# Optimization experiments

Hardware: AMD Instinct MI355X
Metric: run time of the kernel (lower is better)

## Reference

```python
import jax, jax.numpy as jnp
import numpy as np

POOL_SIZES = (1, 3, 6, 8)
EPS = 1e-5


def conv1x1(x, W, b):
    # x: [b, cin, h, w], W: [cout, cin], b: [cout]
    return jnp.einsum('bchw,oc->bohw', x, W) + b[None, :, None, None]


def ppm(x):
    # x: [b, c, h, w] -> [b, c, S] with S = sum(p*p); H,W divisible by each p
    b, c, h, w = x.shape
    outs = []
    for p in POOL_SIZES:
        pooled = x.reshape(b, c, p, h // p, p, w // p).mean(axis=(3, 5))
        outs.append(pooled.reshape(b, c, p * p))
    return jnp.concatenate(outs, axis=-1)


def setup_inputs() -> dict:
    key = jax.random.key(0)
    ks = jax.random.split(key, 8)
    B, Cin, H, W = 4, 512, 120, 120
    Ck, Cv, Cout = 256, 256, 512
    x = jax.random.normal(ks[0], (B, Cin, H, W), dtype=jnp.float32)
    sc = lambda cin: 1.0 / np.sqrt(cin)
    Wk = jax.random.normal(ks[1], (Ck, Cin), dtype=jnp.float32) * sc(Cin)
    bk = jnp.zeros((Ck,), jnp.float32)
    gamma = jnp.ones((Ck,), jnp.float32)
    beta = jnp.zeros((Ck,), jnp.float32)
    mean = jax.random.normal(ks[2], (Ck,), dtype=jnp.float32) * 0.1
    var = jax.random.uniform(ks[3], (Ck,), dtype=jnp.float32, minval=0.5, maxval=1.5)
    Wv = jax.random.normal(ks[4], (Cv, Cin), dtype=jnp.float32) * sc(Cin)
    bv = jnp.zeros((Cv,), jnp.float32)
    # original inits Conv_Out to zero; use random weights for a nontrivial baseline
    Wo = jax.random.normal(ks[5], (Cout, Cv), dtype=jnp.float32) * sc(Cv)
    bo = jnp.zeros((Cout,), jnp.float32)
    return {'x': x, 'Wk': Wk, 'bk': bk, 'gamma': gamma, 'beta': beta,
            'mean': mean, 'var': var, 'Wv': Wv, 'bv': bv, 'Wo': Wo, 'bo': bo}


def reference(x, Wk, bk, gamma, beta, mean, var, Wv, bv, Wo, bo):
    b, _, h, w = x.shape
    ck = Wk.shape[0]
    cv = Wv.shape[0]
    # shared Conv_Key / Conv_Query: conv1x1 -> BN (inference) -> ReLU
    kq = conv1x1(x, Wk, bk)
    inv = gamma / jnp.sqrt(var + EPS)
    kq = jax.nn.relu(kq * inv[None, :, None, None] + (beta - mean * inv)[None, :, None, None])
    value = ppm(conv1x1(x, Wv, bv)).transpose(0, 2, 1)      # [b, S, cv]
    key = ppm(kq)                                            # [b, ck, S]
    query = kq.reshape(b, ck, h * w).transpose(0, 2, 1)      # [b, hw, ck]
    scores = jnp.einsum('bnc,bcs->bns', query, key) * (ck ** -0.5)
    attn = jax.nn.softmax(scores, axis=-1)                   # [b, hw, S]
    agg = jnp.einsum('bns,bsv->bnv', attn, value)            # [b, hw, cv]
    agg = agg.transpose(0, 2, 1).reshape(b, cv, h, w)
    return conv1x1(agg, Wo, bo)
```

## Files before the change

kernel.cpp:

```cpp
#include <hip/hip_runtime.h>
#include <cstdint>
#include <cstddef>

#define HW 14400
#define WIDTH 120
#define S_TOT 110

typedef unsigned short u16;
typedef __attribute__((ext_vector_type(8))) short bf16x8;
typedef __attribute__((ext_vector_type(4))) float f32x4;

__device__ __forceinline__ u16 f2bf(float x) {
  unsigned u = __float_as_uint(x);
  unsigned r = (u + 0x7fffu + ((u >> 16) & 1u)) >> 16;
  return (u16)r;
}
__device__ __forceinline__ float bf2f(u16 h) {
  return __uint_as_float((unsigned)h << 16);
}

__device__ __forceinline__ void async16(void* lds, const void* g) {
  __builtin_amdgcn_global_load_lds(
      (const __attribute__((address_space(1))) void*)g,
      (__attribute__((address_space(3))) void*)lds, 16, 0, 0);
}

__global__ __launch_bounds__(256) void pool_kernel(const float* __restrict__ in,
                                                   float* __restrict__ outp) {
  __shared__ float part[576];
  const float* plane = in + (size_t)blockIdx.x * HW;
  int t = threadIdx.x;
  for (int bb = t; bb < 576; bb += 256) {
    int by = bb / 24, bx = bb % 24;
    const float* p0 = plane + (by * 5) * WIDTH + bx * 5;
    float s = 0.f;
#pragma unroll
    for (int yy = 0; yy < 5; ++yy)
#pragma unroll
      for (int xx = 0; xx < 5; ++xx) s += p0[yy * WIDTH + xx];
    part[bb] = s;
  }
  __syncthreads();
  if (t < S_TOT) {
    float s = 0.f;
    if (t == 0) {
      for (int i = 0; i < 576; ++i) s += part[i];
      s *= (1.f / 14400.f);
    } else if (t < 10) {
      int idx = t - 1, i = idx / 3, j = idx % 3;
      for (int a = 0; a < 8; ++a)
        for (int c = 0; c < 8; ++c) s += part[(i * 8 + a) * 24 + (j * 8 + c)];
      s *= (1.f / 1600.f);
    } else if (t < 46) {
      int idx = t - 10, i = idx / 6, j = idx % 6;
      for (int a = 0; a < 4; ++a)
        for (int c = 0; c < 4; ++c) s += part[(i * 4 + a) * 24 + (j * 4 + c)];
      s *= (1.f / 400.f);
    } else {
      int idx = t - 46, i = idx / 8, j = idx % 8;
      for (int a = 0; a < 3; ++a)
        for (int c = 0; c < 3; ++c) s += part[(i * 3 + a) * 24 + (j * 3 + c)];
      s *= (1.f / 225.f);
    }
    outp[(size_t)blockIdx.x * S_TOT + t] = s;
  }
}

__global__ __launch_bounds__(256) void convert_w(const float* __restrict__ in,
                                                 u16* __restrict__ hi,
                                                 u16* __restrict__ lo, int n) {
  int i = blockIdx.x * 256 + threadIdx.x;
  if (i < n) {
    float v = in[i];
    u16 h = f2bf(v);
    hi[i] = h;
    lo[i] = f2bf(v - bf2f(h));
  }
}

__global__ __launch_bounds__(256) void convert_x(const float* __restrict__ X,
                                                 u16* __restrict__ xth,
                                                 u16* __restrict__ xtl) {
  __shared__ float ls[64][65];
  int b = blockIdx.z;
  int n0 = blockIdx.x * 64, k0 = blockIdx.y * 64;
  int t = threadIdx.x;
  int rt = t >> 4, c4 = (t & 15) * 4;
#pragma unroll
  for (int rr = 0; rr < 4; ++rr) {
    int kk = rr * 16 + rt;
    float4 v = *(const float4*)&X[((size_t)(b * 512 + k0 + kk)) * HW + n0 + c4];
    ls[kk][c4] = v.x; ls[kk][c4 + 1] = v.y; ls[kk][c4 + 2] = v.z; ls[kk][c4 + 3] = v.w;
  }
  __syncthreads();
#pragma unroll
  for (int rr = 0; rr < 4; ++rr) {
    int nn = rr * 16 + rt;
    float v0 = ls[c4 + 0][nn], v1 = ls[c4 + 1][nn], v2 = ls[c4 + 2][nn], v3 = ls[c4 + 3][nn];
    ushort4 oh, ol;
    oh.x = f2bf(v0); ol.x = f2bf(v0 - bf2f(oh.x));
    oh.y = f2bf(v1); ol.y = f2bf(v1 - bf2f(oh.y));
    oh.z = f2bf(v2); ol.z = f2bf(v2 - bf2f(oh.z));
    oh.w = f2bf(v3); ol.w = f2bf(v3 - bf2f(oh.w));
    size_t idx = ((size_t)(b * HW + n0 + nn)) * 512 + k0 + c4;
    *(ushort4*)&xth[idx] = oh;
    *(ushort4*)&xtl[idx] = ol;
  }
}

template <int K, int M_TOT, bool BNRELU>
__global__ __launch_bounds__(256) void gemm_mfma(
    const u16* __restrict__ Ah, const u16* __restrict__ Al,
    const u16* __restrict__ Bh, const u16* __restrict__ Bl,
    float* __restrict__ C,
    const float* __restrict__ p0, const float* __restrict__ p1,
    const float* __restrict__ p2, const float* __restrict__ p3,
    const float* __restrict__ p4) {
  constexpr int NSTEP = K / 32;
  __shared__ alignas(16) u16 sAh[256 * 32];
  __shared__ alignas(16) u16 sAl[256 * 32];
  __shared__ alignas(16) u16 sBh[64 * 32];
  __shared__ alignas(16) u16 sBl[64 * 32];
  __shared__ float sP0[256], sP1[256];

  int t = threadIdx.x, w = t >> 6, l = t & 63;
  int b = blockIdx.z;
  int n0 = blockIdx.x * 64;
  int m0 = blockIdx.y * 256;

  if (BNRELU) {
    int m = m0 + t;
    float iv = p1[m] * rsqrtf(p4[m] + 1e-5f);
    sP0[t] = iv;
    sP1[t] = (p0[m] - p3[m]) * iv + p2[m];
  } else {
    sP0[t] = p0[m0 + t];
  }

  int crow = l >> 2;
  int cbyte = (l & 3) * 16;
  const size_t bOff = (size_t)b * HW;

  f32x4 acc[4][4];
#pragma unroll
  for (int i = 0; i < 4; ++i)
#pragma unroll
    for (int j = 0; j < 4; ++j) acc[i][j] = (f32x4){0.f, 0.f, 0.f, 0.f};

  int fr = l & 15, fk = (l >> 4) * 8;

  for (int ks = 0; ks < NSTEP; ++ks) {
    int k0 = ks * 32;
#pragma unroll
    for (int c = 0; c < 10; ++c) {
      int i = w * 10 + c;
      const u16* g;
      u16* d;
      if (i < 16) {
        g = Ah + (size_t)(m0 + i * 16 + crow) * K + k0;
        d = sAh + i * 512;
      } else if (i < 32) {
        g = Al + (size_t)(m0 + (i - 16) * 16 + crow) * K + k0;
        d = sAl + (i - 16) * 512;
      } else if (i < 36) {
        g = Bh + (bOff + n0 + (i - 32) * 16 + crow) * K + k0;
        d = sBh + (i - 32) * 512;
      } else {
        g = Bl + (bOff + n0 + (i - 36) * 16 + crow) * K + k0;
        d = sBl + (i - 36) * 512;
      }
      async16((char*)d, (const char*)g + cbyte);
    }
    __syncthreads();

    bf16x8 ah[4], al[4], bh[4], bl[4];
#pragma unroll
    for (int mt = 0; mt < 4; ++mt) {
      int r = w * 64 + mt * 16 + fr;
      ah[mt] = *(const bf16x8*)&sAh[r * 32 + fk];
      al[mt] = *(const bf16x8*)&sAl[r * 32 + fk];
    }
#pragma unroll
    for (int nt = 0; nt < 4; ++nt) {
      int r = nt * 16 + fr;
      bh[nt] = *(const bf16x8*)&sBh[r * 32 + fk];
      bl[nt] = *(const bf16x8*)&sBl[r * 32 + fk];
    }
#pragma unroll
    for (int mt = 0; mt < 4; ++mt)
#pragma unroll
      for (int nt = 0; nt < 4; ++nt) {
        acc[mt][nt] = __builtin_amdgcn_mfma_f32_16x16x32_bf16(ah[mt], bh[nt], acc[mt][nt], 0, 0, 0);
        acc[mt][nt] = __builtin_amdgcn_mfma_f32_16x16x32_bf16(ah[mt], bl[nt], acc[mt][nt], 0, 0, 0);
        acc[mt][nt] = __builtin_amdgcn_mfma_f32_16x16x32_bf16(al[mt], bh[nt], acc[mt][nt], 0, 0, 0);
      }
    __syncthreads();
  }

#pragma unroll
  for (int mt = 0; mt < 4; ++mt) {
    int lmBase = w * 64 + mt * 16 + (l >> 4) * 4;
#pragma unroll
    for (int nt = 0; nt < 4; ++nt) {
      int n = n0 + nt * 16 + fr;
#pragma unroll
      for (int r = 0; r < 4; ++r) {
        int lm = lmBase + r;
        float v = acc[mt][nt][r];
        if (BNRELU)
          v = fmaxf(v * sP0[lm] + sP1[lm], 0.f);
        else
          v = v + sP0[lm];
        C[((size_t)(b * M_TOT + m0 + lm)) * HW + n] = v;
      }
    }
  }
}

__global__ __launch_bounds__(256) void value_kernel(
    const float* __restrict__ Wv, const float* __restrict__ xp,
    const float* __restrict__ bv, float* __restrict__ val) {
  int b = blockIdx.x / S_TOT, s = blockIdx.x % S_TOT;
  __shared__ float xs[512];
  int t = threadIdx.x;
  for (int i = t; i < 512; i += 256) xs[i] = xp[((size_t)b * 512 + i) * S_TOT + s];
  __syncthreads();
  float accv = 0.f;
  const float* w = Wv + (size_t)t * 512;
  for (int k = 0; k < 512; k += 4) {
    float4 w4 = *(const float4*)&w[k];
    accv += w4.x * xs[k] + w4.y * xs[k + 1] + w4.z * xs[k + 2] + w4.w * xs[k + 3];
  }
  val[(size_t)blockIdx.x * 256 + t] = accv + bv[t];
}

__global__ __launch_bounds__(256) void attn_kernel(
    const float* __restrict__ kq, const float* __restrict__ keyp,
    const float* __restrict__ value, u16* __restrict__ aggh,
    u16* __restrict__ aggl) {
  __shared__ float sc[64][113];
  __shared__ float qt[32][64];
  __shared__ float kt[32][112];
  __shared__ float red[4][64];
  __shared__ float rinv[64];
  int b = blockIdx.y;
  int pix0 = blockIdx.x * 64;
  int t = threadIdx.x;

  int pi = t & 7;
  int si = t >> 3;
  float a[8][4];
#pragma unroll
  for (int p = 0; p < 8; ++p)
#pragma unroll
    for (int j = 0; j < 4; ++j) a[p][j] = 0.f;

  for (int c0 = 0; c0 < 256; c0 += 32) {
#pragma unroll
    for (int u = 0; u < 2; ++u) {
      int fi = t + u * 256;
      int cc = fi >> 4, p4 = (fi & 15) * 4;
      *(float4*)&qt[cc][p4] =
          *(const float4*)&kq[((size_t)(b * 256 + c0 + cc)) * HW + pix0 + p4];
    }
    for (int i = t; i < 32 * S_TOT; i += 256) {
      int cc = i / S_TOT, ss = i % S_TOT;
      kt[cc][ss] = keyp[((size_t)(b * 256 + c0 + cc)) * S_TOT + ss];
    }
    __syncthreads();
    for (int cc = 0; cc < 32; ++cc) {
      float4 q0 = *(const float4*)&qt[cc][pi * 8];
      float4 q1 = *(const float4*)&qt[cc][pi * 8 + 4];
#pragma unroll
      for (int j = 0; j < 4; ++j) {
        int s = si + 32 * j;
        if (s < S_TOT) {
          float kv = kt[cc][s];
          a[0][j] += q0.x * kv; a[1][j] += q0.y * kv;
          a[2][j] += q0.z * kv; a[3][j] += q0.w * kv;
          a[4][j] += q1.x * kv; a[5][j] += q1.y * kv;
          a[6][j] += q1.z * kv; a[7][j] += q1.w * kv;
        }
      }
    }
    __syncthreads();
  }
#pragma unroll
  for (int j = 0; j < 4; ++j) {
    int s = si + 32 * j;
    if (s < S_TOT) {
#pragma unroll
      for (int p = 0; p < 8; ++p) sc[pi * 8 + p][s] = a[p][j] * 0.0625f;
    }
  }
  __syncthreads();

  int part = t >> 6, r = t & 63;
  int sbeg = part * 28, send = sbeg + 28 < S_TOT ? sbeg + 28 : S_TOT;
  float mx = -1e30f;
  for (int s = sbeg; s < send; ++s) mx = fmaxf(mx, sc[r][s]);
  red[part][r] = mx;
  __syncthreads();
  float m = fmaxf(fmaxf(red[0][r], red[1][r]), fmaxf(red[2][r], red[3][r]));
  float sum = 0.f;
  for (int s = sbeg; s < send; ++s) {
    float e = __expf(sc[r][s] - m);
    sc[r][s] = e;
    sum += e;
  }
  __syncthreads();
  red[part][r] = sum;
  __syncthreads();
  if (part == 0) rinv[r] = 1.f / (red[0][r] + red[1][r] + red[2][r] + red[3][r]);
  __syncthreads();

  int tn2 = t & 63, tm2 = t >> 6;
  int cv = tn2 * 4;
  float4 acc4[16];
#pragma unroll
  for (int p = 0; p < 16; ++p) acc4[p] = make_float4(0.f, 0.f, 0.f, 0.f);
  const float* vb = value + (size_t)b * S_TOT * 256 + cv;
  for (int s = 0; s < S_TOT; ++s) {
    float4 v4 = *(const float4*)&vb[(size_t)s * 256];
#pragma unroll
    for (int p = 0; p < 16; ++p) {
      float e = sc[tm2 * 16 + p][s];
      acc4[p].x += e * v4.x; acc4[p].y += e * v4.y;
      acc4[p].z += e * v4.z; acc4[p].w += e * v4.w;
    }
  }
#pragma unroll
  for (int p = 0; p < 16; ++p) {
    int pix = tm2 * 16 + p;
    float iv = rinv[pix];
    float v0 = acc4[p].x * iv, v1 = acc4[p].y * iv, v2 = acc4[p].z * iv, v3 = acc4[p].w * iv;
    ushort4 oh, ol;
    oh.x = f2bf(v0); ol.x = f2bf(v0 - bf2f(oh.x));
    oh.y = f2bf(v1); ol.y = f2bf(v1 - bf2f(oh.y));
    oh.z = f2bf(v2); ol.z = f2bf(v2 - bf2f(oh.z));
    oh.w = f2bf(v3); ol.w = f2bf(v3 - bf2f(oh.w));
    size_t base = ((size_t)(b * HW + pix0 + pix)) * 256 + cv;
    *(ushort4*)&aggh[base] = oh;
    *(ushort4*)&aggl[base] = ol;
  }
}

extern "C" void kernel_launch(void* const* d_in, const int* in_sizes, int n_in,
                              void* d_out, int out_size, void* d_ws, size_t ws_size,
                              hipStream_t stream) {
  (void)in_sizes; (void)n_in; (void)out_size; (void)ws_size;
  const float* x     = (const float*)d_in[0];
  const float* Wk    = (const float*)d_in[1];
  const float* bk    = (const float*)d_in[2];
  const float* gamma = (const float*)d_in[3];
  const float* beta  = (const float*)d_in[4];
  const float* mean  = (const float*)d_in[5];
  const float* var   = (const float*)d_in[6];
  const float* Wv    = (const float*)d_in[7];
  const float* bv    = (const float*)d_in[8];
  const float* Wo    = (const float*)d_in[9];
  const float* bo    = (const float*)d_in[10];
  float* out = (float*)d_out;

  char* p = (char*)d_ws;
  float* kq = (float*)p;      p += (size_t)14745600 * 4;
  u16* xth = (u16*)p;         p += (size_t)29491200 * 2;
  u16* xtl = (u16*)p;         p += (size_t)29491200 * 2;
  u16* wkh = (u16*)p;         p += 131072 * 2;
  u16* wkl = (u16*)p;         p += 131072 * 2;
  u16* woh = (u16*)p;         p += 131072 * 2;
  u16* wol = (u16*)p;         p += 131072 * 2;
  float* xp = (float*)p;      p += (size_t)4 * 512 * 110 * 4;
  float* value = (float*)p;   p += (size_t)4 * 110 * 256 * 4;
  float* keyp = (float*)p;    p += (size_t)4 * 256 * 110 * 4;
  u16* aggh = xth;
  u16* aggl = xtl;

  convert_w<<<512, 256, 0, stream>>>(Wk, wkh, wkl, 256 * 512);
  convert_w<<<512, 256, 0, stream>>>(Wo, woh, wol, 512 * 256);
  convert_x<<<dim3(225, 8, 4), 256, 0, stream>>>(x, xth, xtl);
  pool_kernel<<<dim3(4 * 512), dim3(256), 0, stream>>>(x, xp);
  value_kernel<<<dim3(4 * S_TOT), dim3(256), 0, stream>>>(Wv, xp, bv, value);
  gemm_mfma<512, 256, true><<<dim3(225, 1, 4), 256, 0, stream>>>(
      wkh, wkl, xth, xtl, kq, bk, gamma, beta, mean, var);
  pool_kernel<<<dim3(4 * 256), dim3(256), 0, stream>>>(kq, keyp);
  attn_kernel<<<dim3(225, 4), 256, 0, stream>>>(kq, keyp, value, aggh, aggl);
  gemm_mfma<256, 512, false><<<dim3(225, 2, 4), 256, 0, stream>>>(
      woh, wol, aggh, aggl, out, bo, nullptr, nullptr, nullptr, nullptr);
}
```

Measured before the change: 645.4 us.

## Rewrite attention with split-bf16 MFMA for scores and value aggregation

Replaces the scalar FP32 attention kernel with an MFMA-based one. Scores and the attention-weighted value sum both use bf16 hi/lo split products (three MFMAs each), and the softmax is done in registers with lane shuffles. New helper kernels transpose kq into bf16 hi/lo pixel-major layout and pad key and value to 128 slots. The extra conversion pass over kq adds memory traffic, and the B operands are read straight from global memory without LDS staging.

New measurement: 619.5 us. 4.0% less time.

```diff
diff --git a/kernel.cpp b/kernel.cpp
--- a/kernel.cpp
+++ b/kernel.cpp
@@ -78,7 +78,8 @@
   }
 }
 
-__global__ __launch_bounds__(256) void convert_x(const float* __restrict__ X,
+template <int CIN>
+__global__ __launch_bounds__(256) void convert_t(const float* __restrict__ X,
                                                  u16* __restrict__ xth,
                                                  u16* __restrict__ xtl) {
   __shared__ float ls[64][65];
@@ -89,7 +90,7 @@
 #pragma unroll
   for (int rr = 0; rr < 4; ++rr) {
     int kk = rr * 16 + rt;
-    float4 v = *(const float4*)&X[((size_t)(b * 512 + k0 + kk)) * HW + n0 + c4];
+    float4 v = *(const float4*)&X[((size_t)(b * CIN + k0 + kk)) * HW + n0 + c4];
     ls[kk][c4] = v.x; ls[kk][c4 + 1] = v.y; ls[kk][c4 + 2] = v.z; ls[kk][c4 + 3] = v.w;
   }
   __syncthreads();
@@ -102,7 +103,7 @@
     oh.y = f2bf(v1); ol.y = f2bf(v1 - bf2f(oh.y));
     oh.z = f2bf(v2); ol.z = f2bf(v2 - bf2f(oh.z));
     oh.w = f2bf(v3); ol.w = f2bf(v3 - bf2f(oh.w));
-    size_t idx = ((size_t)(b * HW + n0 + nn)) * 512 + k0 + c4;
+    size_t idx = ((size_t)(b * HW + n0 + nn)) * CIN + k0 + c4;
     *(ushort4*)&xth[idx] = oh;
     *(ushort4*)&xtl[idx] = ol;
   }
@@ -219,129 +220,161 @@
 
 __global__ __launch_bounds__(256) void value_kernel(
     const float* __restrict__ Wv, const float* __restrict__ xp,
-    const float* __restrict__ bv, float* __restrict__ val) {
-  int b = blockIdx.x / S_TOT, s = blockIdx.x % S_TOT;
+    const float* __restrict__ bv, u16* __restrict__ vth,
+    u16* __restrict__ vtl) {
+  int b = blockIdx.x >> 7, s = blockIdx.x & 127;
+  int t = threadIdx.x;
+  size_t o = ((size_t)(b * 256 + t)) * 128 + s;
+  if (s >= S_TOT) { vth[o] = 0; vtl[o] = 0; return; }
   __shared__ float xs[512];
-  int t = threadIdx.x;
   for (int i = t; i < 512; i += 256) xs[i] = xp[((size_t)b * 512 + i) * S_TOT + s];
   __syncthreads();
   float accv = 0.f;
-  const float* w = Wv + (size_t)t * 512;
+  const float* wv = Wv + (size_t)t * 512;
   for (int k = 0; k < 512; k += 4) {
-    float4 w4 = *(const float4*)&w[k];
+    float4 w4 = *(const float4*)&wv[k];
     accv += w4.x * xs[k] + w4.y * xs[k + 1] + w4.z * xs[k + 2] + w4.w * xs[k + 3];
   }
-  val[(size_t)blockIdx.x * 256 + t] = accv + bv[t];
-}
-
-__global__ __launch_bounds__(256) void attn_kernel(
-    const float* __restrict__ kq, const float* __restrict__ keyp,
-    const float* __restrict__ value, u16* __restrict__ aggh,
-    u16* __restrict__ aggl) {
-  __shared__ float sc[64][113];
-  __shared__ float qt[32][64];
-  __shared__ float kt[32][112];
-  __shared__ float red[4][64];
-  __shared__ float rinv[64];
-  int b = blockIdx.y;
-  int pix0 = blockIdx.x * 64;
+  accv += bv[t];
+  u16 h = f2bf(accv);
+  vth[o] = h;
+  vtl[o] = f2bf(accv - bf2f(h));
+}
+
+__global__ __launch_bounds__(256) void convert_key(const float* __restrict__ keyp,
+                                                   u16* __restrict__ kth,
+                                                   u16* __restrict__ ktl) {
+  int b = blockIdx.x;
   int t = threadIdx.x;
-
-  int pi = t & 7;
-  int si = t >> 3;
-  float a[8][4];
-#pragma unroll
-  for (int p = 0; p < 8; ++p)
-#pragma unroll
-    for (int j = 0; j < 4; ++j) a[p][j] = 0.f;
+  for (int i = t; i < 128 * 256; i += 256) {
+    int s = i >> 8, c = i & 255;
+    float v = (s < S_TOT) ? keyp[((size_t)(b * 256 + c)) * S_TOT + s] : 0.f;
+    u16 h = f2bf(v);
+    size_t o = ((size_t)(b * 128 + s)) * 256 + c;
+    kth[o] = h;
+    ktl[o] = f2bf(v - bf2f(h));
+  }
+}
+
+__global__ __launch_bounds__(256) void attn_mfma(
+    const u16* __restrict__ qh, const u16* __restrict__ ql,
+    const u16* __restrict__ kh, const u16* __restrict__ kl,
+    const u16* __restrict__ vh, const u16* __restrict__ vl,
+    u16* __restrict__ aggh, u16* __restrict__ aggl) {
+  __shared__ u16 Ph[64][136];
+  __shared__ u16 Pl[64][136];
+  int b = blockIdx.y, pix0 = blockIdx.x * 64;
+  int t = threadIdx.x, w = t >> 6, l = t & 63;
+  int fr = l & 15, q = l >> 4, fk = q * 8;
+
+  f32x4 acc[7];
+#pragma unroll
+  for (int st = 0; st < 7; ++st) acc[st] = (f32x4){0.f, 0.f, 0.f, 0.f};
+
+  const u16* qbh = qh + ((size_t)(b * HW + pix0 + w * 16 + fr)) * 256 + fk;
+  const u16* qbl = ql + ((size_t)(b * HW + pix0 + w * 16 + fr)) * 256 + fk;
+  const u16* kbh = kh + ((size_t)(b * 128 + fr)) * 256 + fk;
+  const u16* kbl = kl + ((size_t)(b * 128 + fr)) * 256 + fk;
 
   for (int c0 = 0; c0 < 256; c0 += 32) {
-#pragma unroll
-    for (int u = 0; u < 2; ++u) {
-      int fi = t + u * 256;
-      int cc = fi >> 4, p4 = (fi & 15) * 4;
-      *(float4*)&qt[cc][p4] =
-          *(const float4*)&kq[((size_t)(b * 256 + c0 + cc)) * HW + pix0 + p4];
-    }
-    for (int i = t; i < 32 * S_TOT; i += 256) {
-      int cc = i / S_TOT, ss = i % S_TOT;
-      kt[cc][ss] = keyp[((size_t)(b * 256 + c0 + cc)) * S_TOT + ss];
-    }
-    __syncthreads();
-    for (int cc = 0; cc < 32; ++cc) {
-      float4 q0 = *(const float4*)&qt[cc][pi * 8];
-      float4 q1 = *(const float4*)&qt[cc][pi * 8 + 4];
-#pragma unroll
-      for (int j = 0; j < 4; ++j) {
-        int s = si + 32 * j;
-        if (s < S_TOT) {
-          float kv = kt[cc][s];
-          a[0][j] += q0.x * kv; a[1][j] += q0.y * kv;
-          a[2][j] += q0.z * kv; a[3][j] += q0.w * kv;
-          a[4][j] += q1.x * kv; a[5][j] += q1.y * kv;
-          a[6][j] += q1.z * kv; a[7][j] += q1.w * kv;
-        }
-      }
-    }
-    __syncthreads();
-  }
-#pragma unroll
-  for (int j = 0; j < 4; ++j) {
-    int s = si + 32 * j;
-    if (s < S_TOT) {
-#pragma unroll
-      for (int p = 0; p < 8; ++p) sc[pi * 8 + p][s] = a[p][j] * 0.0625f;
-    }
+    bf16x8 ah = *(const bf16x8*)(qbh + c0);
+    bf16x8 al = *(const bf16x8*)(qbl + c0);
+#pragma unroll
+    for (int st = 0; st < 7; ++st) {
+      bf16x8 bh = *(const bf16x8*)(kbh + (size_t)st * 16 * 256 + c0);
+      bf16x8 bl = *(const bf16x8*)(kbl + (size_t)st * 16 * 256 + c0);
+      acc[st] = __builtin_amdgcn_mfma_f32_16x16x32_bf16(ah, bh, acc[st], 0, 0, 0);
+      acc[st] = __builtin_amdgcn_mfma_f32_16x16x32_bf16(ah, bl, acc[st], 0, 0, 0);
+      acc[st] = __builtin_amdgcn_mfma_f32_16x16x32_bf16(al, bh, acc[st], 0, 0, 0);
+    }
+  }
+
+#pragma unroll
+  for (int st = 0; st < 7; ++st)
+#pragma unroll
+    for (int r = 0; r < 4; ++r) acc[st][r] *= 0.0625f;
+  if (fr >= 14) {
+#pragma unroll
+    for (int r = 0; r < 4; ++r) acc[6][r] = -1e30f;
+  }
+
+#pragma unroll
+  for (int r = 0; r < 4; ++r) {
+    float m = -1e30f;
+#pragma unroll
+    for (int st = 0; st < 7; ++st) m = fmaxf(m, acc[st][r]);
+    m = fmaxf(m, __shfl_xor(m, 1));
+    m = fmaxf(m, __shfl_xor(m, 2));
+    m = fmaxf(m, __shfl_xor(m, 4));
+    m = fmaxf(m, __shfl_xor(m, 8));
+    float s = 0.f;
+#pragma unroll
+    for (int st = 0; st < 7; ++st) {
+      float e = __expf(acc[st][r] - m);
+      acc[st][r] = e;
+      s += e;
+    }
+    s += __shfl_xor(s, 1);
+    s += __shfl_xor(s, 2);
+    s += __shfl_xor(s, 4);
+    s += __shfl_xor(s, 8);
+    float inv = 1.f / s;
+#pragma unroll
+    for (int st = 0; st < 7; ++st) acc[st][r] *= inv;
+  }
+
+  int prow = w * 16 + q * 4;
+#pragma unroll
+  for (int st = 0; st < 7; ++st) {
+    int s = st * 16 + fr;
+#pragma unroll
+    for (int r = 0; r < 4; ++r) {
+      float v = acc[st][r];
+      u16 h = f2bf(v);
+      Ph[prow + r][s] = h;
+      Pl[prow + r][s] = f2bf(v - bf2f(h));
+    }
+  }
+  for (int i = t; i < 64 * 16; i += 256) {
+    int rr = i >> 4, ss = 112 + (i & 15);
+    Ph[rr][ss] = 0;
+    Pl[rr][ss] = 0;
   }
   __syncthreads();
 
-  int part = t >> 6, r = t & 63;
-  int sbeg = part * 28, send = sbeg + 28 < S_TOT ? sbeg + 28 : S_TOT;
-  float mx = -1e30f;
-  for (int s = sbeg; s < send; ++s) mx = fmaxf(mx, sc[r][s]);
-  red[part][r] = mx;
-  __syncthreads();
-  float m = fmaxf(fmaxf(red[0][r], red[1][r]), fmaxf(red[2][r], red[3][r]));
-  float sum = 0.f;
-  for (int s = sbeg; s < send; ++s) {
-    float e = __expf(sc[r][s] - m);
-    sc[r][s] = e;
-    sum += e;
-  }
-  __syncthreads();
-  red[part][r] = sum;
-  __syncthreads();
-  if (part == 0) rinv[r] = 1.f / (red[0][r] + red[1][r] + red[2][r] + red[3][r]);
-  __syncthreads();
-
-  int tn2 = t & 63, tm2 = t >> 6;
-  int cv = tn2 * 4;
-  float4 acc4[16];
-#pragma unroll
-  for (int p = 0; p < 16; ++p) acc4[p] = make_float4(0.f, 0.f, 0.f, 0.f);
-  const float* vb = value + (size_t)b * S_TOT * 256 + cv;
-  for (int s = 0; s < S_TOT; ++s) {
-    float4 v4 = *(const float4*)&vb[(size_t)s * 256];
-#pragma unroll
-    for (int p = 0; p < 16; ++p) {
-      float e = sc[tm2 * 16 + p][s];
-      acc4[p].x += e * v4.x; acc4[p].y += e * v4.y;
-      acc4[p].z += e * v4.z; acc4[p].w += e * v4.w;
-    }
-  }
-#pragma unroll
-  for (int p = 0; p < 16; ++p) {
-    int pix = tm2 * 16 + p;
-    float iv = rinv[pix];
-    float v0 = acc4[p].x * iv, v1 = acc4[p].y * iv, v2 = acc4[p].z * iv, v3 = acc4[p].w * iv;
-    ushort4 oh, ol;
-    oh.x = f2bf(v0); ol.x = f2bf(v0 - bf2f(oh.x));
-    oh.y = f2bf(v1); ol.y = f2bf(v1 - bf2f(oh.y));
-    oh.z = f2bf(v2); ol.z = f2bf(v2 - bf2f(oh.z));
-    oh.w = f2bf(v3); ol.w = f2bf(v3 - bf2f(oh.w));
-    size_t base = ((size_t)(b * HW + pix0 + pix)) * 256 + cv;
-    *(ushort4*)&aggh[base] = oh;
-    *(ushort4*)&aggl[base] = ol;
+  f32x4 oacc[16];
+#pragma unroll
+  for (int nt = 0; nt < 16; ++nt) oacc[nt] = (f32x4){0.f, 0.f, 0.f, 0.f};
+
+  const u16* vbh = vh + ((size_t)(b * 256 + fr)) * 128 + fk;
+  const u16* vbl = vl + ((size_t)(b * 256 + fr)) * 128 + fk;
+
+#pragma unroll
+  for (int kc = 0; kc < 4; ++kc) {
+    bf16x8 ah = *(const bf16x8*)&Ph[w * 16 + fr][kc * 32 + fk];
+    bf16x8 al = *(const bf16x8*)&Pl[w * 16 + fr][kc * 32 + fk];
+#pragma unroll
+    for (int nt = 0; nt < 16; ++nt) {
+      bf16x8 bh = *(const bf16x8*)(vbh + (size_t)nt * 16 * 128 + kc * 32);
+      bf16x8 bl = *(const bf16x8*)(vbl + (size_t)nt * 16 * 128 + kc * 32);
+      oacc[nt] = __builtin_amdgcn_mfma_f32_16x16x32_bf16(ah, bh, oacc[nt], 0, 0, 0);
+      oacc[nt] = __builtin_amdgcn_mfma_f32_16x16x32_bf16(ah, bl, oacc[nt], 0, 0, 0);
+      oacc[nt] = __builtin_amdgcn_mfma_f32_16x16x32_bf16(al, bh, oacc[nt], 0, 0, 0);
+    }
+  }
+
+#pragma unroll
+  for (int nt = 0; nt < 16; ++nt) {
+    int cv = nt * 16 + fr;
+#pragma unroll
+    for (int r = 0; r < 4; ++r) {
+      int pix = pix0 + w * 16 + q * 4 + r;
+      float v = oacc[nt][r];
+      u16 h = f2bf(v);
+      size_t o = ((size_t)(b * HW + pix)) * 256 + cv;
+      aggh[o] = h;
+      aggl[o] = f2bf(v - bf2f(h));
+    }
   }
 }
 
@@ -371,20 +404,28 @@
   u16* woh = (u16*)p;         p += 131072 * 2;
   u16* wol = (u16*)p;         p += 131072 * 2;
   float* xp = (float*)p;      p += (size_t)4 * 512 * 110 * 4;
-  float* value = (float*)p;   p += (size_t)4 * 110 * 256 * 4;
   float* keyp = (float*)p;    p += (size_t)4 * 256 * 110 * 4;
+  u16* vth = (u16*)p;         p += (size_t)4 * 256 * 128 * 2;
+  u16* vtl = (u16*)p;         p += (size_t)4 * 256 * 128 * 2;
+  u16* kth = (u16*)p;         p += (size_t)4 * 128 * 256 * 2;
+  u16* ktl = (u16*)p;         p += (size_t)4 * 128 * 256 * 2;
   u16* aggh = xth;
+  u16* kqth = xth + (size_t)14745600;
   u16* aggl = xtl;
+  u16* kqtl = xtl + (size_t)14745600;
 
   convert_w<<<512, 256, 0, stream>>>(Wk, wkh, wkl, 256 * 512);
   convert_w<<<512, 256, 0, stream>>>(Wo, woh, wol, 512 * 256);
-  convert_x<<<dim3(225, 8, 4), 256, 0, stream>>>(x, xth, xtl);
+  convert_t<512><<<dim3(225, 8, 4), 256, 0, stream>>>(x, xth, xtl);
   pool_kernel<<<dim3(4 * 512), dim3(256), 0, stream>>>(x, xp);
-  value_kernel<<<dim3(4 * S_TOT), dim3(256), 0, stream>>>(Wv, xp, bv, value);
+  value_kernel<<<dim3(4 * 128), dim3(256), 0, stream>>>(Wv, xp, bv, vth, vtl);
   gemm_mfma<512, 256, true><<<dim3(225, 1, 4), 256, 0, stream>>>(
       wkh, wkl, xth, xtl, kq, bk, gamma, beta, mean, var);
+  convert_t<256><<<dim3(225, 4, 4), 256, 0, stream>>>(kq, kqth, kqtl);
   pool_kernel<<<dim3(4 * 256), dim3(256), 0, stream>>>(kq, keyp);
-  attn_kernel<<<dim3(225, 4), 256, 0, stream>>>(kq, keyp, value, aggh, aggl);
+  convert_key<<<dim3(4), dim3(256), 0, stream>>>(keyp, kth, ktl);
+  attn_mfma<<<dim3(225, 4), 256, 0, stream>>>(kqth, kqtl, kth, ktl, vth, vtl,
+                                              aggh, aggl);
   gemm_mfma<256, 512, false><<<dim3(225, 2, 4), 256, 0, stream>>>(
       woh, wol, aggh, aggl, out, bo, nullptr, nullptr, nullptr, nullptr);
 }
```
